# Kernel optimization log

Measured on AMD Instinct MI355X. Metric: run time of the kernel, lower is better.

## Reference

```python
import jax, jax.numpy as jnp
import numpy as np

NY, NU, NH = 8, 8, 256
T, NB = 2048, 64


def setup_inputs() -> dict:
    key = jax.random.key(0)
    ks = jax.random.split(key, 10)
    return {
        "_y0": jax.random.normal(ks[0], (NB, NY), dtype=jnp.float32),
        "_U": jax.random.normal(ks[1], (T, NB, NU), dtype=jnp.float32),
        "lmbd_cont_real": jax.random.uniform(ks[2], (NH // 2,), dtype=jnp.float32),
        "lmbd_cont_imag": jax.random.uniform(ks[3], (NH // 2,), dtype=jnp.float32),
        "B": jax.random.normal(ks[4], (NH, NU), dtype=jnp.float32) / np.sqrt(NU).astype(np.float32),
        "multiplier_on_B": jnp.zeros((NH,), dtype=jnp.float32),
        "W_y2x": jax.random.normal(ks[5], (NH, NY), dtype=jnp.float32) / np.sqrt(NY).astype(np.float32),
        "b_y2x": jax.random.normal(ks[6], (NH,), dtype=jnp.float32) * 0.01,
        "W_x2y": jax.random.normal(ks[7], (NY, NH), dtype=jnp.float32) / np.sqrt(NH).astype(np.float32),
        "b_x2y": jax.random.normal(ks[8], (NY,), dtype=jnp.float32) * 0.01,
    }


def reference(_y0, _U, lmbd_cont_real, lmbd_cont_imag, B, multiplier_on_B,
              W_y2x, b_y2x, W_x2y, b_x2y):
    H2 = lmbd_cont_real.shape[0]
    # input drive: (T, NB, NH)
    Bu = jnp.einsum('tbu,hu->tbh', _U, B) * jnp.exp(multiplier_on_B)
    # stable complex-conjugate-pair eigenvalues
    r = jnp.exp(-jnp.abs(lmbd_cont_real))
    theta = (jnp.pi / 2) * lmbd_cont_imag
    re = r * jnp.cos(theta)
    im = r * jnp.sin(theta)
    # initial state from y0
    x0 = _y0 @ W_y2x.T + b_y2x  # (NB, NH)

    def step(x, bu):
        x1, x2 = x[:, :H2], x[:, H2:]
        # A = [[diag(re), -diag(im)], [diag(im), diag(re)]]; x <- x A^T + bu
        nx = jnp.concatenate([re * x1 - im * x2, im * x1 + re * x2], axis=1) + bu
        return nx, nx

    _, X = jax.lax.scan(step, x0, Bu)  # X: (T, NB, NH)
    Y = X @ W_x2y.T + b_x2y  # (T, NB, NY)
    return Y
```

## Files before the change

kernel.cpp:

```cpp
#include <hip/hip_runtime.h>
#include <math.h>

#define T_   2048
#define NB_  64
#define NU_  8
#define NY_  8
#define NH_  256
#define H2_  128
#define CCH  64
#define LCH  32

static const float PI_HALF = 1.5707963267948966f;

typedef _Float16 half8  __attribute__((ext_vector_type(8)));
typedef __fp16   fp16x2 __attribute__((ext_vector_type(2)));
typedef float    f32x4  __attribute__((ext_vector_type(4)));


__global__ __launch_bounds__(128) void k_scanproj(
    const float* __restrict__ U, const float* __restrict__ lr,
    const float* __restrict__ li, const float* __restrict__ B,
    const float* __restrict__ mult, const float* __restrict__ Wx2y,
    const float* __restrict__ bx2y, float* __restrict__ c_buf,
    float* __restrict__ Y)
{
    const int k   = blockIdx.x >> 6;
    const int b   = blockIdx.x & 63;
    const int tid = threadIdx.x;
    const int h   = tid;
    const int w   = tid >> 6;
    const int l   = tid & 63;
    const int row = l & 15;
    const int kg  = (l >> 4) & 3;

    float rr = expf(-fabsf(lr[h]));
    float th = PI_HALF * li[h];
    float re = rr * cosf(th), im = rr * sinf(th);

    float B1[NU_], B2[NU_];
    {
        float s1 = expf(mult[h]), s2 = expf(mult[h+H2_]);
        float4 b1a = *(const float4*)(B + h*NU_);
        float4 b1b = *(const float4*)(B + h*NU_ + 4);
        float4 b2a = *(const float4*)(B + (h+H2_)*NU_);
        float4 b2b = *(const float4*)(B + (h+H2_)*NU_ + 4);
        B1[0]=b1a.x*s1; B1[1]=b1a.y*s1; B1[2]=b1a.z*s1; B1[3]=b1a.w*s1;
        B1[4]=b1b.x*s1; B1[5]=b1b.y*s1; B1[6]=b1b.z*s1; B1[7]=b1b.w*s1;
        B2[0]=b2a.x*s2; B2[1]=b2a.y*s2; B2[2]=b2a.z*s2; B2[3]=b2a.w*s2;
        B2[4]=b2b.x*s2; B2[5]=b2b.y*s2; B2[6]=b2b.z*s2; B2[7]=b2b.w*s2;
    }

    half8 wf[4];
    #pragma unroll
    for (int q2 = 0; q2 < 4; q2++) {
        const int q = 4*w + q2;
        union { uint32_t u32[4]; half8 h8; } fu;
        if (row < 8) {
            const int hh = q*16 + kg*4;
            const float* lo = Wx2y + row*NH_ + hh;
            const float* hi = lo + H2_;
            #pragma unroll
            for (int i = 0; i < 4; i++) {
                union { fp16x2 h2; uint32_t u; } pk;
                pk.h2 = __builtin_amdgcn_cvt_pkrtz(lo[i], hi[i]);
                fu.u32[i] = pk.u;
            }
        } else {
            fu.u32[0]=0; fu.u32[1]=0; fu.u32[2]=0; fu.u32[3]=0;
        }
        wf[q2] = fu.h8;
    }
    const float bias = bx2y[tid & 7];

    __shared__ float    uS[LCH*NU_];
    __shared__ _Float16 xS[16*256];
    __shared__ float    pS[4*132];
    uint32_t* xS32 = (uint32_t*)xS;

    if (tid < 64) {
        ((float4*)uS)[tid] =
            *(const float4*)(U + ((size_t)(k*LCH + (tid>>1))*NB_ + b)*NU_ + (tid&1)*4);
    }
    __syncthreads();

    float x1 = 0.f, x2 = 0.f;
    const int g = h >> 2;

    for (int s = 0; s < 2; s++) {
        #pragma unroll 4
        for (int t16 = 0; t16 < 16; t16++) {
            const int t = s*16 + t16;
            float4 u0 = ((const float4*)uS)[2*t+0];
            float4 u1 = ((const float4*)uS)[2*t+1];
            float u[NU_] = {u0.x,u0.y,u0.z,u0.w,u1.x,u1.y,u1.z,u1.w};
            float bu1=0.f, bu2=0.f;
            #pragma unroll
            for (int i = 0; i < NU_; i++) {
                bu1 = fmaf(u[i], B1[i], bu1);
                bu2 = fmaf(u[i], B2[i], bu2);
            }
            float n1 = fmaf(re, x1, fmaf(-im, x2, bu1));
            float n2 = fmaf(im, x1, fmaf( re, x2, bu2));
            x1 = n1; x2 = n2;

            union { fp16x2 h2; uint32_t u32; } pk;
            pk.h2 = __builtin_amdgcn_cvt_pkrtz(x1, x2);
            xS32[t16*128 + ((g ^ t16) & 31)*4 + (h & 3)] = pk.u32;
        }
        __syncthreads();

        f32x4 acc = {0.f,0.f,0.f,0.f};
        #pragma unroll
        for (int q2 = 0; q2 < 4; q2++) {
            const int q = 4*w + q2;
            const int p = ((q << 2) + kg) ^ row;
            const half8* ap = (const half8*)(xS + (row << 8) + (p << 3));
            acc = __builtin_amdgcn_mfma_f32_16x16x32_f16(*ap, wf[q2], acc, 0, 0, 0);
        }
        #pragma unroll
        for (int r = 0; r < 4; r++) pS[r*132 + w*64 + l] = acc[r];
        __syncthreads();

        {
            const int t  = tid >> 3, y = tid & 7;
            const int ls = ((t >> 2) << 4) + y;
            const int rg = t & 3;
            float sum = pS[rg*132 + ls] + pS[rg*132 + 64 + ls];
            Y[((size_t)(k*LCH + s*16 + t)*NB_ + b)*NY_ + y] = sum + bias;
        }
    }

    *(float2*)(c_buf + (size_t)(k*NB_ + b)*(H2_*2) + 2*h) = make_float2(x1, x2);
}

__global__ __launch_bounds__(64) void k_mid(
    const float* __restrict__ y0, const float* __restrict__ lr,
    const float* __restrict__ li, const float* __restrict__ Wy2x,
    const float* __restrict__ by2x, const float* __restrict__ Wx2y,
    const float* __restrict__ c_buf, uint32_t* __restrict__ initT,
    uint32_t* __restrict__ M32)
{
    const int bi = blockIdx.x;
    const int j  = threadIdx.x;

    if (bi < 128) {
        const int gidx = bi*64 + j;
        const int b = gidx >> 7;
        const int h = gidx & 127;

        float x1 = by2x[h], x2 = by2x[h+H2_];
        #pragma unroll
        for (int y = 0; y < NY_; y++) {
            float yy = y0[b*NY_ + y];
            x1 = fmaf(yy, Wy2x[h*NY_ + y],        x1);
            x2 = fmaf(yy, Wy2x[(h+H2_)*NY_ + y],  x2);
        }

        float rL  = expf(-(float)LCH * fabsf(lr[h]));
        float thL = (float)LCH * PI_HALF * li[h];
        float reL = rL * cosf(thL), imL = rL * sinf(thL);

        #pragma unroll 8
        for (int k = 0; k < CCH; k++) {
            float2 c = *(const float2*)(c_buf + (size_t)k*16384 + b*256 + 2*h);
            union { fp16x2 hh; uint32_t u32; } pk;
            pk.hh = __builtin_amdgcn_cvt_pkrtz(x1, x2);
            initT[(size_t)k*8192 + b*128 + h] = pk.u32;
            float n1 = fmaf(reL, x1, fmaf(-imL, x2, c.x));
            float n2 = fmaf(imL, x1, fmaf( reL, x2, c.y));
            x1 = n1; x2 = n2;
        }
    } else {
        const int R = bi - 128;
        const int dlt = R >> 3, y = R & 7;
        const float e = (float)(dlt + 1);
        #pragma unroll
        for (int hh = 0; hh < 2; hh++) {
            const int h = j + hh*64;
            float r  = expf(-e * fabsf(lr[h]));
            float an = e * PI_HALF * li[h];
            float c = r * cosf(an), sn = r * sinf(an);
            float W1 = Wx2y[y*NH_ + h];
            float W2 = Wx2y[y*NH_ + h + H2_];
            float Mre = fmaf(W1, c,  W2 * sn);
            float Mim = fmaf(W2, c, -W1 * sn);
            union { fp16x2 h2; uint32_t u32; } pk;
            pk.h2 = __builtin_amdgcn_cvt_pkrtz(Mre, Mim);
            M32[R*128 + hh*64 + j] = pk.u32;
        }
    }
}

__global__ __launch_bounds__(256) void k_corr(
    const _Float16* __restrict__ M, const uint32_t* __restrict__ initT,
    float* __restrict__ Y)
{
    const int k    = blockIdx.x >> 1;
    const int half = blockIdx.x & 1;
    const int tid  = threadIdx.x;
    const int w    = tid >> 6, l = tid & 63;
    const int lane16 = l & 15, kg = l >> 4;

    __shared__ _Float16 bS[32*264];
    {
        uint32_t* bS32 = (uint32_t*)bS;
        const int r = tid >> 3, seg = tid & 7;
        const uint32_t* src = initT + (size_t)k*8192 + (half*32 + r)*128 + seg*16;
        uint32_t* dst = bS32 + r*132 + seg*16;
        ((uint4*)dst)[0] = ((const uint4*)src)[0];
        ((uint4*)dst)[1] = ((const uint4*)src)[1];
        ((uint4*)dst)[2] = ((const uint4*)src)[2];
        ((uint4*)dst)[3] = ((const uint4*)src)[3];
    }
    __syncthreads();

    #pragma unroll
    for (int rt = 0; rt < 4; rt++) {
        const int R0 = w*64 + rt*16;
        half8 af[8];
        #pragma unroll
        for (int q = 0; q < 8; q++)
            af[q] = *(const half8*)(M + (size_t)(R0 + lane16)*256 + q*32 + kg*8);

        f32x4 acc0 = {0.f,0.f,0.f,0.f}, acc1 = {0.f,0.f,0.f,0.f};
        #pragma unroll
        for (int q = 0; q < 8; q++) {
            const half8* b0 = (const half8*)(bS + ( 0 + lane16)*264 + q*32 + kg*8);
            const half8* b1 = (const half8*)(bS + (16 + lane16)*264 + q*32 + kg*8);
            acc0 = __builtin_amdgcn_mfma_f32_16x16x32_f16(af[q], *b0, acc0, 0, 0, 0);
            acc1 = __builtin_amdgcn_mfma_f32_16x16x32_f16(af[q], *b1, acc1, 0, 0, 0);
        }

        const int t  = k*LCH + (R0 >> 3) + (kg >> 1);
        const int y0 = (kg & 1) * 4;
        float4* yp0 = (float4*)(Y + ((size_t)t*NB_ + half*32 +  0 + lane16)*NY_ + y0);
        float4* yp1 = (float4*)(Y + ((size_t)t*NB_ + half*32 + 16 + lane16)*NY_ + y0);
        float4 o0 = *yp0, o1 = *yp1;
        o0.x += acc0[0]; o0.y += acc0[1]; o0.z += acc0[2]; o0.w += acc0[3];
        o1.x += acc1[0]; o1.y += acc1[1]; o1.z += acc1[2]; o1.w += acc1[3];
        *yp0 = o0; *yp1 = o1;
    }
}

extern "C" void kernel_launch(void* const* d_in, const int* in_sizes, int n_in,
                              void* d_out, int out_size, void* d_ws, size_t ws_size,
                              hipStream_t stream) {
    const float* y0   = (const float*)d_in[0];
    const float* U    = (const float*)d_in[1];
    const float* lr   = (const float*)d_in[2];
    const float* li   = (const float*)d_in[3];
    const float* B    = (const float*)d_in[4];
    const float* mult = (const float*)d_in[5];
    const float* Wy2x = (const float*)d_in[6];
    const float* by2x = (const float*)d_in[7];
    const float* Wx2y = (const float*)d_in[8];
    const float* bx2y = (const float*)d_in[9];
    float* Y = (float*)d_out;

    uint32_t* Mbuf  = (uint32_t*)d_ws;
    float*    c_buf = (float*)((char*)d_ws + (128<<10));
    uint32_t* initT = (uint32_t*)((char*)d_ws + (128<<10) + (4<<20));

    k_scanproj<<<CCH*NB_, 128, 0, stream>>>(U, lr, li, B, mult, Wx2y, bx2y, c_buf, Y);
    k_mid     <<<384, 64, 0, stream>>>(y0, lr, li, Wy2x, by2x, Wx2y, c_buf, initT, Mbuf);
    k_corr    <<<CCH*2, 256, 0, stream>>>((const _Float16*)Mbuf, initT, Y);
}
```

Measured before the change: 104.5 us.

## Hoist parameter precompute into prologue kernel and widen correction grid

Adds a small prologue kernel that computes eigenvalue coefficients, exp-scaled B, the fp16-packed output weights and the M matrix once, so the 4096 scan blocks load them instead of each recomputing expf/cos/sin and repacking. The mid kernel becomes a pure prefix over chunk carries. The correction kernel's grid grows fourfold, with each block handling one row tile instead of looping over four, to fill more CUs. This costs an extra kernel launch and some redundant LDS staging of initT per block.

Measured after the change: 102.6 us, median of 2. About the same (-1.8%).

```diff
diff --git a/kernel.cpp b/kernel.cpp
--- a/kernel.cpp
+++ b/kernel.cpp
@@ -16,12 +16,86 @@
 typedef __fp16   fp16x2 __attribute__((ext_vector_type(2)));
 typedef float    f32x4  __attribute__((ext_vector_type(4)));
 
+#define OFF_LAMP  0
+#define OFF_LAML  2048
+#define OFF_BS    4096
+#define OFF_WM16  12288
+#define OFF_M     16384
+#define OFF_CBUF  147456
+#define OFF_INIT  4341760
+
+__global__ __launch_bounds__(64) void k_pre(
+    const float* __restrict__ lr, const float* __restrict__ li,
+    const float* __restrict__ B, const float* __restrict__ mult,
+    const float* __restrict__ Wx2y, char* __restrict__ ws)
+{
+    const int bi = blockIdx.x;
+    const int j  = threadIdx.x;
+
+    if (bi < 256) {
+        uint32_t* M32 = (uint32_t*)(ws + OFF_M);
+        const int dlt = bi >> 3, y = bi & 7;
+        const float e = (float)(dlt + 1);
+        #pragma unroll
+        for (int hh = 0; hh < 2; hh++) {
+            const int h = j + hh*64;
+            float r  = expf(-e * fabsf(lr[h]));
+            float an = e * PI_HALF * li[h];
+            float c = r * cosf(an), sn = r * sinf(an);
+            float W1 = Wx2y[y*NH_ + h];
+            float W2 = Wx2y[y*NH_ + h + H2_];
+            float Mre = fmaf(W1, c,  W2 * sn);
+            float Mim = fmaf(W2, c, -W1 * sn);
+            union { fp16x2 h2; uint32_t u32; } pk;
+            pk.h2 = __builtin_amdgcn_cvt_pkrtz(Mre, Mim);
+            M32[bi*128 + hh*64 + j] = pk.u32;
+        }
+    } else if (bi == 256) {
+        float4* lamP = (float4*)(ws + OFF_LAMP);
+        float2* lamL = (float2*)(ws + OFF_LAML);
+        #pragma unroll
+        for (int hh = 0; hh < 2; hh++) {
+            const int h = j + hh*64;
+            float a  = fabsf(lr[h]);
+            float r  = expf(-a);
+            float th = PI_HALF * li[h];
+            float re = r * cosf(th), im = r * sinf(th);
+            lamP[h] = make_float4(re, im, -im, re);
+            float rL  = expf(-(float)LCH * a);
+            float thL = (float)LCH * PI_HALF * li[h];
+            lamL[h] = make_float2(rL * cosf(thL), rL * sinf(thL));
+        }
+    } else if (bi == 257) {
+        float* Bs = (float*)(ws + OFF_BS);
+        #pragma unroll
+        for (int hh = 0; hh < 2; hh++) {
+            const int h = j + hh*64;
+            float s1 = expf(mult[h]), s2 = expf(mult[h+H2_]);
+            #pragma unroll
+            for (int i = 0; i < NU_; i++) {
+                Bs[h*16 + i]     = B[h*NU_ + i]        * s1;
+                Bs[h*16 + 8 + i] = B[(h+H2_)*NU_ + i]  * s2;
+            }
+        }
+    } else {
+        uint32_t* Wm = (uint32_t*)(ws + OFF_WM16);
+        #pragma unroll
+        for (int y = 0; y < NY_; y++) {
+            #pragma unroll
+            for (int hh = 0; hh < 2; hh++) {
+                const int h = j + hh*64;
+                union { fp16x2 h2; uint32_t u32; } pk;
+                pk.h2 = __builtin_amdgcn_cvt_pkrtz(Wx2y[y*NH_ + h],
+                                                   Wx2y[y*NH_ + h + H2_]);
+                Wm[y*128 + h] = pk.u32;
+            }
+        }
+    }
+}
 
 __global__ __launch_bounds__(128) void k_scanproj(
-    const float* __restrict__ U, const float* __restrict__ lr,
-    const float* __restrict__ li, const float* __restrict__ B,
-    const float* __restrict__ mult, const float* __restrict__ Wx2y,
-    const float* __restrict__ bx2y, float* __restrict__ c_buf,
+    const float* __restrict__ U, const float* __restrict__ bx2y,
+    const char* __restrict__ ws, float* __restrict__ c_buf,
     float* __restrict__ Y)
 {
     const int k   = blockIdx.x >> 6;
@@ -33,42 +107,27 @@
     const int row = l & 15;
     const int kg  = (l >> 4) & 3;
 
-    float rr = expf(-fabsf(lr[h]));
-    float th = PI_HALF * li[h];
-    float re = rr * cosf(th), im = rr * sinf(th);
-
+    const float4 lam = ((const float4*)(ws + OFF_LAMP))[h];
     float B1[NU_], B2[NU_];
     {
-        float s1 = expf(mult[h]), s2 = expf(mult[h+H2_]);
-        float4 b1a = *(const float4*)(B + h*NU_);
-        float4 b1b = *(const float4*)(B + h*NU_ + 4);
-        float4 b2a = *(const float4*)(B + (h+H2_)*NU_);
-        float4 b2b = *(const float4*)(B + (h+H2_)*NU_ + 4);
-        B1[0]=b1a.x*s1; B1[1]=b1a.y*s1; B1[2]=b1a.z*s1; B1[3]=b1a.w*s1;
-        B1[4]=b1b.x*s1; B1[5]=b1b.y*s1; B1[6]=b1b.z*s1; B1[7]=b1b.w*s1;
-        B2[0]=b2a.x*s2; B2[1]=b2a.y*s2; B2[2]=b2a.z*s2; B2[3]=b2a.w*s2;
-        B2[4]=b2b.x*s2; B2[5]=b2b.y*s2; B2[6]=b2b.z*s2; B2[7]=b2b.w*s2;
-    }
-
+        const float4* bsp = (const float4*)(ws + OFF_BS) + h*4;
+        float4 a0 = bsp[0], a1 = bsp[1], a2 = bsp[2], a3 = bsp[3];
+        B1[0]=a0.x; B1[1]=a0.y; B1[2]=a0.z; B1[3]=a0.w;
+        B1[4]=a1.x; B1[5]=a1.y; B1[6]=a1.z; B1[7]=a1.w;
+        B2[0]=a2.x; B2[1]=a2.y; B2[2]=a2.z; B2[3]=a2.w;
+        B2[4]=a3.x; B2[5]=a3.y; B2[6]=a3.z; B2[7]=a3.w;
+    }
     half8 wf[4];
-    #pragma unroll
-    for (int q2 = 0; q2 < 4; q2++) {
-        const int q = 4*w + q2;
-        union { uint32_t u32[4]; half8 h8; } fu;
-        if (row < 8) {
-            const int hh = q*16 + kg*4;
-            const float* lo = Wx2y + row*NH_ + hh;
-            const float* hi = lo + H2_;
-            #pragma unroll
-            for (int i = 0; i < 4; i++) {
-                union { fp16x2 h2; uint32_t u; } pk;
-                pk.h2 = __builtin_amdgcn_cvt_pkrtz(lo[i], hi[i]);
-                fu.u32[i] = pk.u;
-            }
-        } else {
-            fu.u32[0]=0; fu.u32[1]=0; fu.u32[2]=0; fu.u32[3]=0;
-        }
-        wf[q2] = fu.h8;
+    {
+        const uint32_t* Wm = (const uint32_t*)(ws + OFF_WM16);
+        #pragma unroll
+        for (int q2 = 0; q2 < 4; q2++) {
+            const int q = 4*w + q2;
+            union { uint4 u4; half8 h8; } fu;
+            if (row < 8) fu.u4 = *(const uint4*)(Wm + row*128 + q*16 + kg*4);
+            else         fu.u4 = make_uint4(0,0,0,0);
+            wf[q2] = fu.h8;
+        }
     }
     const float bias = bx2y[tid & 7];
 
@@ -99,8 +158,8 @@
                 bu1 = fmaf(u[i], B1[i], bu1);
                 bu2 = fmaf(u[i], B2[i], bu2);
             }
-            float n1 = fmaf(re, x1, fmaf(-im, x2, bu1));
-            float n2 = fmaf(im, x1, fmaf( re, x2, bu2));
+            float n1 = fmaf(lam.x, x1, fmaf(lam.z, x2, bu1));
+            float n2 = fmaf(lam.y, x1, fmaf(lam.w, x2, bu2));
             x1 = n1; x2 = n2;
 
             union { fp16x2 h2; uint32_t u32; } pk;
@@ -133,61 +192,35 @@
     *(float2*)(c_buf + (size_t)(k*NB_ + b)*(H2_*2) + 2*h) = make_float2(x1, x2);
 }
 
-__global__ __launch_bounds__(64) void k_mid(
-    const float* __restrict__ y0, const float* __restrict__ lr,
-    const float* __restrict__ li, const float* __restrict__ Wy2x,
-    const float* __restrict__ by2x, const float* __restrict__ Wx2y,
-    const float* __restrict__ c_buf, uint32_t* __restrict__ initT,
-    uint32_t* __restrict__ M32)
+__global__ __launch_bounds__(64) void k_prefix(
+    const float* __restrict__ y0, const float* __restrict__ Wy2x,
+    const float* __restrict__ by2x, const char* __restrict__ ws,
+    const float* __restrict__ c_buf, uint32_t* __restrict__ initT)
 {
-    const int bi = blockIdx.x;
-    const int j  = threadIdx.x;
-
-    if (bi < 128) {
-        const int gidx = bi*64 + j;
-        const int b = gidx >> 7;
-        const int h = gidx & 127;
-
-        float x1 = by2x[h], x2 = by2x[h+H2_];
-        #pragma unroll
-        for (int y = 0; y < NY_; y++) {
-            float yy = y0[b*NY_ + y];
-            x1 = fmaf(yy, Wy2x[h*NY_ + y],        x1);
-            x2 = fmaf(yy, Wy2x[(h+H2_)*NY_ + y],  x2);
-        }
-
-        float rL  = expf(-(float)LCH * fabsf(lr[h]));
-        float thL = (float)LCH * PI_HALF * li[h];
-        float reL = rL * cosf(thL), imL = rL * sinf(thL);
-
-        #pragma unroll 8
-        for (int k = 0; k < CCH; k++) {
-            float2 c = *(const float2*)(c_buf + (size_t)k*16384 + b*256 + 2*h);
-            union { fp16x2 hh; uint32_t u32; } pk;
-            pk.hh = __builtin_amdgcn_cvt_pkrtz(x1, x2);
-            initT[(size_t)k*8192 + b*128 + h] = pk.u32;
-            float n1 = fmaf(reL, x1, fmaf(-imL, x2, c.x));
-            float n2 = fmaf(imL, x1, fmaf( reL, x2, c.y));
-            x1 = n1; x2 = n2;
-        }
-    } else {
-        const int R = bi - 128;
-        const int dlt = R >> 3, y = R & 7;
-        const float e = (float)(dlt + 1);
-        #pragma unroll
-        for (int hh = 0; hh < 2; hh++) {
-            const int h = j + hh*64;
-            float r  = expf(-e * fabsf(lr[h]));
-            float an = e * PI_HALF * li[h];
-            float c = r * cosf(an), sn = r * sinf(an);
-            float W1 = Wx2y[y*NH_ + h];
-            float W2 = Wx2y[y*NH_ + h + H2_];
-            float Mre = fmaf(W1, c,  W2 * sn);
-            float Mim = fmaf(W2, c, -W1 * sn);
-            union { fp16x2 h2; uint32_t u32; } pk;
-            pk.h2 = __builtin_amdgcn_cvt_pkrtz(Mre, Mim);
-            M32[R*128 + hh*64 + j] = pk.u32;
-        }
+    const int g = blockIdx.x*64 + threadIdx.x;
+    const int b = g >> 7;
+    const int h = g & 127;
+
+    float x1 = by2x[h], x2 = by2x[h+H2_];
+    #pragma unroll
+    for (int y = 0; y < NY_; y++) {
+        float yy = y0[b*NY_ + y];
+        x1 = fmaf(yy, Wy2x[h*NY_ + y],        x1);
+        x2 = fmaf(yy, Wy2x[(h+H2_)*NY_ + y],  x2);
+    }
+
+    const float2 lL = ((const float2*)(ws + OFF_LAML))[h];
+    const float reL = lL.x, imL = lL.y;
+
+    #pragma unroll 8
+    for (int k = 0; k < CCH; k++) {
+        float2 c = *(const float2*)(c_buf + (size_t)k*16384 + b*256 + 2*h);
+        union { fp16x2 hh; uint32_t u32; } pk;
+        pk.hh = __builtin_amdgcn_cvt_pkrtz(x1, x2);
+        initT[(size_t)k*8192 + b*128 + h] = pk.u32;
+        float n1 = fmaf(reL, x1, fmaf(-imL, x2, c.x));
+        float n2 = fmaf(imL, x1, fmaf( reL, x2, c.y));
+        x1 = n1; x2 = n2;
     }
 }
 
@@ -195,8 +228,10 @@
     const _Float16* __restrict__ M, const uint32_t* __restrict__ initT,
     float* __restrict__ Y)
 {
-    const int k    = blockIdx.x >> 1;
-    const int half = blockIdx.x & 1;
+    const int bi   = blockIdx.x;
+    const int k    = bi >> 3;
+    const int half = (bi >> 2) & 1;
+    const int rtg  = bi & 3;
     const int tid  = threadIdx.x;
     const int w    = tid >> 6, l = tid & 63;
     const int lane16 = l & 15, kg = l >> 4;
@@ -214,32 +249,29 @@
     }
     __syncthreads();
 
+    const int R0 = rtg*64 + w*16;
+    half8 af[8];
     #pragma unroll
-    for (int rt = 0; rt < 4; rt++) {
-        const int R0 = w*64 + rt*16;
-        half8 af[8];
-        #pragma unroll
-        for (int q = 0; q < 8; q++)
-            af[q] = *(const half8*)(M + (size_t)(R0 + lane16)*256 + q*32 + kg*8);
-
-        f32x4 acc0 = {0.f,0.f,0.f,0.f}, acc1 = {0.f,0.f,0.f,0.f};
-        #pragma unroll
-        for (int q = 0; q < 8; q++) {
-            const half8* b0 = (const half8*)(bS + ( 0 + lane16)*264 + q*32 + kg*8);
-            const half8* b1 = (const half8*)(bS + (16 + lane16)*264 + q*32 + kg*8);
-            acc0 = __builtin_amdgcn_mfma_f32_16x16x32_f16(af[q], *b0, acc0, 0, 0, 0);
-            acc1 = __builtin_amdgcn_mfma_f32_16x16x32_f16(af[q], *b1, acc1, 0, 0, 0);
-        }
-
-        const int t  = k*LCH + (R0 >> 3) + (kg >> 1);
-        const int y0 = (kg & 1) * 4;
-        float4* yp0 = (float4*)(Y + ((size_t)t*NB_ + half*32 +  0 + lane16)*NY_ + y0);
-        float4* yp1 = (float4*)(Y + ((size_t)t*NB_ + half*32 + 16 + lane16)*NY_ + y0);
-        float4 o0 = *yp0, o1 = *yp1;
-        o0.x += acc0[0]; o0.y += acc0[1]; o0.z += acc0[2]; o0.w += acc0[3];
-        o1.x += acc1[0]; o1.y += acc1[1]; o1.z += acc1[2]; o1.w += acc1[3];
-        *yp0 = o0; *yp1 = o1;
-    }
+    for (int q = 0; q < 8; q++)
+        af[q] = *(const half8*)(M + (size_t)(R0 + lane16)*256 + q*32 + kg*8);
+
+    f32x4 acc0 = {0.f,0.f,0.f,0.f}, acc1 = {0.f,0.f,0.f,0.f};
+    #pragma unroll
+    for (int q = 0; q < 8; q++) {
+        const half8* b0 = (const half8*)(bS + ( 0 + lane16)*264 + q*32 + kg*8);
+        const half8* b1 = (const half8*)(bS + (16 + lane16)*264 + q*32 + kg*8);
+        acc0 = __builtin_amdgcn_mfma_f32_16x16x32_f16(af[q], *b0, acc0, 0, 0, 0);
+        acc1 = __builtin_amdgcn_mfma_f32_16x16x32_f16(af[q], *b1, acc1, 0, 0, 0);
+    }
+
+    const int t  = k*LCH + (R0 >> 3) + (kg >> 1);
+    const int y0 = (kg & 1) * 4;
+    float4* yp0 = (float4*)(Y + ((size_t)t*NB_ + half*32 +  0 + lane16)*NY_ + y0);
+    float4* yp1 = (float4*)(Y + ((size_t)t*NB_ + half*32 + 16 + lane16)*NY_ + y0);
+    float4 o0 = *yp0, o1 = *yp1;
+    o0.x += acc0[0]; o0.y += acc0[1]; o0.z += acc0[2]; o0.w += acc0[3];
+    o1.x += acc1[0]; o1.y += acc1[1]; o1.z += acc1[2]; o1.w += acc1[3];
+    *yp0 = o0; *yp1 = o1;
 }
 
 extern "C" void kernel_launch(void* const* d_in, const int* in_sizes, int n_in,
@@ -257,11 +289,13 @@
     const float* bx2y = (const float*)d_in[9];
     float* Y = (float*)d_out;
 
-    uint32_t* Mbuf  = (uint32_t*)d_ws;
-    float*    c_buf = (float*)((char*)d_ws + (128<<10));
-    uint32_t* initT = (uint32_t*)((char*)d_ws + (128<<10) + (4<<20));
-
-    k_scanproj<<<CCH*NB_, 128, 0, stream>>>(U, lr, li, B, mult, Wx2y, bx2y, c_buf, Y);
-    k_mid     <<<384, 64, 0, stream>>>(y0, lr, li, Wy2x, by2x, Wx2y, c_buf, initT, Mbuf);
-    k_corr    <<<CCH*2, 256, 0, stream>>>((const _Float16*)Mbuf, initT, Y);
-}
+    char*     ws    = (char*)d_ws;
+    float*    c_buf = (float*)(ws + OFF_CBUF);
+    uint32_t* initT = (uint32_t*)(ws + OFF_INIT);
+    const _Float16* Mf = (const _Float16*)(ws + OFF_M);
+
+    k_pre     <<<259, 64, 0, stream>>>(lr, li, B, mult, Wx2y, ws);
+    k_scanproj<<<CCH*NB_, 128, 0, stream>>>(U, bx2y, ws, c_buf, Y);
+    k_prefix  <<<(NB_*H2_)/64, 64, 0, stream>>>(y0, Wy2x, by2x, ws, c_buf, initT);
+    k_corr    <<<CCH*8, 256, 0, stream>>>(Mf, initT, Y);
+}
```
